# Optimization experiments

Measured on AMD Instinct MI355X. Metric: run time of the kernel, lower is better.

## Reference

```python
import jax, jax.numpy as jnp
import numpy as np

B, S, D_MODEL = 2, 1024, 3072
HEADS, HEAD_DIM = 24, 128
EPS = 1e-6


def _rms_norm(x, w):
    # RMSNorm over last dim (head_dim), elementwise affine
    var = jnp.mean(jnp.square(x), axis=-1, keepdims=True)
    return x * jax.lax.rsqrt(var + EPS) * w


def _apply_rotary(x, freqs_cis):
    # x: [B, S, H, D]; freqs_cis: [S, 1, rot_dim] broadcasting over B via leading dims
    rot_dim = freqs_cis.shape[-1]
    xr, x_pass = x[..., :rot_dim], x[..., rot_dim:]
    cos_ = jnp.cos(freqs_cis).astype(x.dtype)
    sin_ = jnp.sin(freqs_cis).astype(x.dtype)
    x1, x2 = jnp.split(xr, 2, axis=-1)
    x_rot = jnp.concatenate((-x2, x1), axis=-1)
    return jnp.concatenate((xr * cos_ + x_rot * sin_, x_pass), axis=-1)


def setup_inputs() -> dict:
    key = jax.random.key(0)
    ks = jax.random.split(key, 8)
    inner = HEADS * HEAD_DIM
    scale = 1.0 / np.sqrt(D_MODEL)
    return {
        "hidden_states": jax.random.normal(ks[0], (B, S, D_MODEL), dtype=jnp.float32),
        "image_rotary_emb": jax.random.uniform(ks[1], (S, 1, HEAD_DIM), dtype=jnp.float32) * 6.283,
        "Wq": jax.random.normal(ks[2], (inner, D_MODEL), dtype=jnp.float32) * scale,
        "Wk": jax.random.normal(ks[3], (inner, D_MODEL), dtype=jnp.float32) * scale,
        "Wv": jax.random.normal(ks[4], (inner, D_MODEL), dtype=jnp.float32) * scale,
        "Wo": jax.random.normal(ks[5], (D_MODEL, inner), dtype=jnp.float32) * scale,
        "norm_q_w": jnp.ones((HEAD_DIM,), dtype=jnp.float32),
        "norm_k_w": jnp.ones((HEAD_DIM,), dtype=jnp.float32),
    }


def reference(hidden_states, image_rotary_emb, Wq, Wk, Wv, Wo, norm_q_w, norm_k_w):
    # QKV projections: [B,S,Dm] @ [Dm,inner] -> [B,S,H,Dh]
    q = jnp.einsum("bsd,ed->bse", hidden_states, Wq).reshape(B, S, HEADS, HEAD_DIM)
    k = jnp.einsum("bsd,ed->bse", hidden_states, Wk).reshape(B, S, HEADS, HEAD_DIM)
    v = jnp.einsum("bsd,ed->bse", hidden_states, Wv).reshape(B, S, HEADS, HEAD_DIM)
    # per-head RMSNorm on q/k
    q = _rms_norm(q, norm_q_w)
    k = _rms_norm(k, norm_k_w)
    # RoPE (Megatron rotate_half, full head dim rotated)
    q = _apply_rotary(q, image_rotary_emb)
    k = _apply_rotary(k, image_rotary_emb)
    # SDPA (non-causal, no mask): [B,H,S,S]
    scale = 1.0 / np.sqrt(HEAD_DIM)
    scores = jnp.einsum("bqhd,bkhd->bhqk", q, k) * scale
    attn = jax.nn.softmax(scores, axis=-1)
    out = jnp.einsum("bhqk,bkhd->bqhd", attn, v).reshape(B, S, HEADS * HEAD_DIM)
    return jnp.einsum("bse,de->bsd", out, Wo)
```

## Files before the change

### kernel.cpp

```cpp
#include <hip/hip_runtime.h>
#include <hip/hip_bf16.h>
#include <math.h>

#define B_   2
#define S_   1024
#define DM_  3072
#define H_   24
#define HD_  128
#define BH_  (B_*H_)
#define KDIM 3072
#define QSCALE 0.08838834764831845f

typedef __attribute__((ext_vector_type(8))) short short8;
typedef __attribute__((ext_vector_type(4))) float f32x4;

__device__ __forceinline__ unsigned short f2bf(float f) {
    union { float f; unsigned u; } v; v.f = f;
    unsigned r = v.u + 0x7fffu + ((v.u >> 16) & 1u);
    return (unsigned short)(r >> 16);
}

#define GLD_LDS16(gptr, ldsptr)                                                            \
    __builtin_amdgcn_global_load_lds(                                                      \
        (const __attribute__((address_space(1))) unsigned int*)(gptr),                     \
        (__attribute__((address_space(3))) unsigned int*)(ldsptr), 16, 0, 0)

#define SEG0 1572864
#define SEGW 2359296
#define SB1  (SEG0 + SEGW)
#define SB2  (SB1 + SEGW)
#define SB3  (SB2 + SEGW)
#define SB4  (SB3 + SEGW)
#define SB5  (SB4 + 32768)
#define CVT_BLOCKS 43136

__global__ __launch_bounds__(256) void cvt_all(const float* __restrict__ hs,
                                               const float* __restrict__ Wq,
                                               const float* __restrict__ Wk,
                                               const float* __restrict__ Wv,
                                               const float* __restrict__ Wo,
                                               const float* __restrict__ freqs,
                                               unsigned short* __restrict__ Xb,
                                               unsigned short* __restrict__ Wqkvb,
                                               unsigned short* __restrict__ Wob,
                                               float2* __restrict__ tab) {
    int i = blockIdx.x * 256 + threadIdx.x;
    const float* src;
    unsigned short* dst;
    int j;
    if (i < SEG0)      { src = hs; dst = Xb;              j = i; }
    else if (i < SB1)  { src = Wq; dst = Wqkvb;           j = i - SEG0; }
    else if (i < SB2)  { src = Wk; dst = Wqkvb + 9437184; j = i - SB1; }
    else if (i < SB3)  { src = Wv; dst = Wqkvb + 18874368; j = i - SB2; }
    else if (i < SB4)  { src = Wo; dst = Wob;             j = i - SB3; }
    else {
        j = i - SB4;
        float4 f = ((const float4*)freqs)[j];
        float4 lo = make_float4(cosf(f.x), sinf(f.x), cosf(f.y), sinf(f.y));
        float4 hi = make_float4(cosf(f.z), sinf(f.z), cosf(f.w), sinf(f.w));
        ((float4*)tab)[2 * j]     = lo;
        ((float4*)tab)[2 * j + 1] = hi;
        return;
    }
    float4 v = ((const float4*)src)[j];
    ushort4 o;
    o.x = f2bf(v.x); o.y = f2bf(v.y); o.z = f2bf(v.z); o.w = f2bf(v.w);
    ((ushort4*)dst)[j] = o;
}

template <int FUSED>
__global__ __launch_bounds__(256) void gemm_fused(const unsigned short* __restrict__ A,
                                                  const unsigned short* __restrict__ Bm,
                                                  float* __restrict__ C, int Ndim,
                                                  const float2* __restrict__ rtab,
                                                  const float* __restrict__ nqw,
                                                  const float* __restrict__ nkw,
                                                  unsigned short* __restrict__ Qb,
                                                  unsigned short* __restrict__ Kb,
                                                  unsigned short* __restrict__ Vtb) {
    __shared__ __align__(16) unsigned short As[128 * 64];
    __shared__ __align__(16) unsigned short Bs[128 * 64];
    __shared__ float pse[4][64];
    const int t = threadIdx.x;
    const int bx = blockIdx.x;
    const int m0 = blockIdx.y * 128, n0 = bx * 128;
    const int w = t >> 6, lane = t & 63, quad = lane >> 4, ln = lane & 15;
    const int wm = (w >> 1) * 64;
    const int p = w & 1;
    const int dj0 = p ? 32 : 0;
    const int rl = lane >> 3;
    const int gc = (lane & 7) ^ rl;
    const int cs = ln & 7;
    const int woff = (w == 1) ? 32 : (w == 2) ? -32 : 0;

    f32x4 acc[4][4];
#pragma unroll
    for (int i = 0; i < 4; ++i)
#pragma unroll
        for (int j = 0; j < 4; ++j) acc[i][j] = (f32x4){0.f, 0.f, 0.f, 0.f};

    const unsigned short* ga = &A[(long long)(m0 + w * 32 + rl) * KDIM + gc * 8];
    const unsigned short* gb = &Bm[(long long)(n0 + w * 32 + woff + rl) * KDIM + gc * 8];

    for (int kt = 0; kt < KDIM / 64; ++kt) {
#pragma unroll
        for (int c = 0; c < 4; ++c) {
            const int r0 = w * 32 + c * 8;
            GLD_LDS16(ga + (long long)(c * 8) * KDIM, &As[r0 * 64]);
            GLD_LDS16(gb + (long long)(c * 8) * KDIM, &Bs[r0 * 64]);
        }
        ga += 64; gb += 64;
        __syncthreads();
#pragma unroll
        for (int ks = 0; ks < 2; ++ks) {
            short8 a[4], b[4];
#pragma unroll
            for (int i = 0; i < 4; ++i) {
                int row = wm + i * 16 + ln;
                a[i] = *(const short8*)&As[row * 64 + (((ks * 4 + quad) ^ cs) << 3)];
            }
#pragma unroll
            for (int j = 0; j < 4; ++j) {
                int row = p * 64 + j * 16 + ln;
                b[j] = *(const short8*)&Bs[row * 64 + (((ks * 4 + quad) ^ cs) << 3)];
            }
#pragma unroll
            for (int i = 0; i < 4; ++i)
#pragma unroll
                for (int j = 0; j < 4; ++j)
                    acc[i][j] = __builtin_amdgcn_mfma_f32_16x16x32_bf16(a[i], b[j], acc[i][j], 0, 0, 0);
        }
        __syncthreads();
    }

    if (!FUSED) {
#pragma unroll
        for (int i = 0; i < 4; ++i)
#pragma unroll
            for (int reg = 0; reg < 4; ++reg) {
                int row = m0 + wm + i * 16 + quad * 4 + reg;
                float* crow = C + (long long)row * Ndim + n0 + ln;
                crow[dj0]      = acc[i][0][reg];
                crow[dj0 + 16] = acc[i][1][reg];
                crow[dj0 + 64] = acc[i][2][reg];
                crow[dj0 + 80] = acc[i][3][reg];
            }
        return;
    }
    const int region = bx / 24;
    const int h = bx % 24;
    if (region < 2) {
#pragma unroll
        for (int i = 0; i < 4; ++i)
#pragma unroll
            for (int reg = 0; reg < 4; ++reg) {
                float s = 0.f;
#pragma unroll
                for (int j = 0; j < 4; ++j) { float v = acc[i][j][reg]; s += v * v; }
#pragma unroll
                for (int off = 8; off; off >>= 1) s += __shfl_xor(s, off, 16);
                if (ln == 0) pse[w][i * 16 + quad * 4 + reg] = s;
            }
        __syncthreads();
        const float* nw = region ? nkw : nqw;
        unsigned short* outp = region ? Kb : Qb;
        const float scl = region ? 1.f : QSCALE;
        const float nw0  = nw[dj0 + ln],      nw1  = nw[dj0 + 16 + ln];
        const float nw64 = nw[dj0 + 64 + ln], nw80 = nw[dj0 + 80 + ln];
#pragma unroll
        for (int i = 0; i < 4; ++i)
#pragma unroll
            for (int reg = 0; reg < 4; ++reg) {
                const int idx = i * 16 + quad * 4 + reg;
                const float tot = pse[w][idx] + pse[w ^ 1][idx];
                const float rr = rsqrtf(tot * (1.f / 128.f) + 1e-6f);
                const int row = m0 + wm + idx;
                const int b = row >> 10, s = row & 1023;
                const long long ob = ((long long)(b * H_ + h) * S_ + s) * HD_;
                {
                    const int d1 = dj0 + ln;
                    float y1 = acc[i][0][reg] * rr * nw0;
                    float y2 = acc[i][2][reg] * rr * nw64;
                    float2 c1 = rtab[s * HD_ + d1], c2 = rtab[s * HD_ + d1 + 64];
                    outp[ob + d1]      = f2bf((y1 * c1.x - y2 * c1.y) * scl);
                    outp[ob + d1 + 64] = f2bf((y2 * c2.x + y1 * c2.y) * scl);
                }
                {
                    const int d1 = dj0 + 16 + ln;
                    float y1 = acc[i][1][reg] * rr * nw1;
                    float y2 = acc[i][3][reg] * rr * nw80;
                    float2 c1 = rtab[s * HD_ + d1], c2 = rtab[s * HD_ + d1 + 64];
                    outp[ob + d1]      = f2bf((y1 * c1.x - y2 * c1.y) * scl);
                    outp[ob + d1 + 64] = f2bf((y2 * c2.x + y1 * c2.y) * scl);
                }
            }
    } else {
#pragma unroll
        for (int i = 0; i < 4; ++i)
#pragma unroll
            for (int reg = 0; reg < 4; ++reg) {
                const int row = m0 + wm + i * 16 + quad * 4 + reg;
                const int b = row >> 10, s = row & 1023;
                const long long vb = (long long)(b * H_ + h) * HD_;
#pragma unroll
                for (int j = 0; j < 4; ++j) {
                    const int d = dj0 + (j & 1) * 16 + (j >> 1) * 64 + ln;
                    Vtb[(vb + d) * S_ + s] = f2bf(acc[i][j][reg]);
                }
            }
    }
}

__global__ __launch_bounds__(256) void attn(const unsigned short* __restrict__ Qb,
                                            const unsigned short* __restrict__ Kb,
                                            const unsigned short* __restrict__ Vtb,
                                            unsigned short* __restrict__ Ob) {
    __shared__ __align__(16) unsigned short Ks[64 * 128];
    __shared__ __align__(16) unsigned short Vts[128 * 64];
    __shared__ __align__(16) unsigned short Ps[4][16][72];
    const int bh = blockIdx.x, qt = blockIdx.y;
    const int t = threadIdx.x, w = t >> 6, lane = t & 63, quad = lane >> 4, ln = lane & 15;
    const int b = bh / H_, h = bh - b * H_;

    short8 qfrag[4];
    const long long qbase = ((long long)bh * S_ + qt * 64 + w * 16 + ln) * HD_;
#pragma unroll
    for (int ks = 0; ks < 4; ++ks)
        qfrag[ks] = *(const short8*)&Qb[qbase + ks * 32 + quad * 8];

    f32x4 o[8];
#pragma unroll
    for (int n = 0; n < 8; ++n) o[n] = (f32x4){0.f, 0.f, 0.f, 0.f};
    float l_run[4] = {0.f, 0.f, 0.f, 0.f};

    const int krow_l = lane >> 4, ksl = lane & 15;
    const int vrow_l = lane >> 3, vsl = lane & 7;

    for (int kt = 0; kt < S_ / 64; ++kt) {
        __syncthreads();
#pragma unroll
        for (int c = 0; c < 4; ++c) {
            {
                const int r = c * 16 + w * 4 + krow_l;
                const int gcn = ksl ^ (r & 15);
                GLD_LDS16(&Kb[((long long)bh * S_ + kt * 64 + r) * HD_ + gcn * 8],
                          &Ks[(c * 16 + w * 4) * 128]);
            }
            {
                const int r = c * 32 + w * 8 + vrow_l;
                const int gcn = vsl ^ (r & 7);
                GLD_LDS16(&Vtb[((long long)bh * HD_ + r) * S_ + kt * 64 + gcn * 8],
                          &Vts[(c * 32 + w * 8) * 64]);
            }
        }
        __syncthreads();
        f32x4 sj[4];
#pragma unroll
        for (int j = 0; j < 4; ++j) {
            f32x4 sa = (f32x4){0.f, 0.f, 0.f, 0.f};
#pragma unroll
            for (int ks = 0; ks < 4; ++ks) {
                const int row = j * 16 + ln;
                const int slot = (ks * 4 + quad) ^ (row & 15);
                short8 bb = *(const short8*)&Ks[row * 128 + slot * 8];
                sa = __builtin_amdgcn_mfma_f32_16x16x32_bf16(qfrag[ks], bb, sa, 0, 0, 0);
            }
            sj[j] = sa;
        }
#pragma unroll
        for (int r = 0; r < 4; ++r) {
            float sum = 0.f;
#pragma unroll
            for (int j = 0; j < 4; ++j) {
                float p = __expf(sj[j][r]);
                sj[j][r] = p;
                sum += p;
            }
#pragma unroll
            for (int off = 8; off; off >>= 1) sum += __shfl_xor(sum, off, 16);
            l_run[r] += sum;
        }
#pragma unroll
        for (int j = 0; j < 4; ++j)
#pragma unroll
            for (int r = 0; r < 4; ++r)
                Ps[w][quad * 4 + r][j * 16 + ln] = f2bf(sj[j][r]);
        __asm__ volatile("s_waitcnt lgkmcnt(0)" ::: "memory");
#pragma unroll
        for (int ks = 0; ks < 2; ++ks) {
            short8 pf = *(const short8*)&Ps[w][ln][ks * 32 + quad * 8];
#pragma unroll
            for (int n = 0; n < 8; ++n) {
                const int row = n * 16 + ln;
                const int slot = (ks * 4 + quad) ^ (row & 7);
                short8 vf = *(const short8*)&Vts[row * 64 + slot * 8];
                o[n] = __builtin_amdgcn_mfma_f32_16x16x32_bf16(pf, vf, o[n], 0, 0, 0);
            }
        }
    }
    float inv[4];
#pragma unroll
    for (int r = 0; r < 4; ++r) inv[r] = 1.f / l_run[r];
    const int row_s = qt * 64 + w * 16 + quad * 4;
#pragma unroll
    for (int n = 0; n < 8; ++n)
#pragma unroll
        for (int r = 0; r < 4; ++r) {
            long long off = ((long long)b * S_ + row_s + r) * DM_ + h * HD_ + n * 16 + ln;
            Ob[off] = f2bf(o[n][r] * inv[r]);
        }
}

extern "C" void kernel_launch(void* const* d_in, const int* in_sizes, int n_in,
                              void* d_out, int out_size, void* d_ws, size_t ws_size,
                              hipStream_t stream) {
    const float* hs    = (const float*)d_in[0];
    const float* freqs = (const float*)d_in[1];
    const float* Wq    = (const float*)d_in[2];
    const float* Wk    = (const float*)d_in[3];
    const float* Wv    = (const float*)d_in[4];
    const float* Wo    = (const float*)d_in[5];
    const float* nqw   = (const float*)d_in[6];
    const float* nkw   = (const float*)d_in[7];
    float* out = (float*)d_out;

    char* ws = (char*)d_ws;
    unsigned short* Xb    = (unsigned short*)(ws);
    unsigned short* Wqkvb = (unsigned short*)(ws + 12582912LL);
    unsigned short* Wob   = (unsigned short*)(ws + 69206016LL);
    unsigned short* Qb    = (unsigned short*)(ws + 88080384LL);
    unsigned short* Kb    = (unsigned short*)(ws + 100663296LL);
    unsigned short* Vtb   = (unsigned short*)(ws + 113246208LL);
    unsigned short* Ob    = (unsigned short*)(ws + 125829120LL);
    float2*         rtab  = (float2*)        (ws + 138412032LL);

    cvt_all<<<CVT_BLOCKS, 256, 0, stream>>>(hs, Wq, Wk, Wv, Wo, freqs,
                                            Xb, Wqkvb, Wob, rtab);
    gemm_fused<1><<<dim3(72, 16), 256, 0, stream>>>(Xb, Wqkvb, nullptr, 0,
                                                    rtab, nqw, nkw, Qb, Kb, Vtb);
    attn<<<dim3(BH_, S_ / 64), 256, 0, stream>>>(Qb, Kb, Vtb, Ob);
    gemm_fused<0><<<dim3(24, 16), 256, 0, stream>>>(Ob, Wob, out, DM_,
                                                    nullptr, nullptr, nullptr,
                                                    nullptr, nullptr, nullptr);
}
```

Before: 459.5 us.

## Double-buffer attention K/V tiles and stage GEMM epilogue stores through LDS

The attention kernel now double-buffers its K and V^T shared-memory tiles. It issues the async global-to-LDS loads for the next key tile before computing on the current one, and raises wave priority around the MFMA sections. The QKV GEMM epilogue writes normalized and rotated Q/K, and transposed V, into a swizzled LDS tile that reuses the GEMM's staging memory. It then emits coalesced 16-byte global stores instead of scattered 2-byte stores, the V^T layout being the worst case. The cost is doubled attention LDS footprint, which may lower occupancy, and an extra barrier. In the V path the reuse of shared memory has no barrier before the writes, so it depends on all warps having finished reading the GEMM tiles.

After: 466.3 us. About the same (+1.5%).

```diff
diff --git a/kernel.cpp b/kernel.cpp
--- a/kernel.cpp
+++ b/kernel.cpp
@@ -78,9 +78,10 @@
                                                   unsigned short* __restrict__ Qb,
                                                   unsigned short* __restrict__ Kb,
                                                   unsigned short* __restrict__ Vtb) {
-    __shared__ __align__(16) unsigned short As[128 * 64];
-    __shared__ __align__(16) unsigned short Bs[128 * 64];
+    __shared__ __align__(16) unsigned short smem[128 * 128];
     __shared__ float pse[4][64];
+    unsigned short* const As = smem;
+    unsigned short* const Bs = smem + 128 * 64;
     const int t = threadIdx.x;
     const int bx = blockIdx.x;
     const int m0 = blockIdx.y * 128, n0 = bx * 128;
@@ -149,6 +150,10 @@
     }
     const int region = bx / 24;
     const int h = bx % 24;
+    unsigned short* const Ct = smem;
+    const int bb  = m0 >> 10;
+    const int s0g = m0 & 1023;
+
     if (region < 2) {
 #pragma unroll
         for (int i = 0; i < 4; ++i)
@@ -174,40 +179,56 @@
                 const int idx = i * 16 + quad * 4 + reg;
                 const float tot = pse[w][idx] + pse[w ^ 1][idx];
                 const float rr = rsqrtf(tot * (1.f / 128.f) + 1e-6f);
-                const int row = m0 + wm + idx;
-                const int b = row >> 10, s = row & 1023;
-                const long long ob = ((long long)(b * H_ + h) * S_ + s) * HD_;
+                const int rloc = wm + idx;
+                const int s = s0g + rloc;
+                const int sw = (rloc & 15) << 3;
                 {
                     const int d1 = dj0 + ln;
                     float y1 = acc[i][0][reg] * rr * nw0;
                     float y2 = acc[i][2][reg] * rr * nw64;
                     float2 c1 = rtab[s * HD_ + d1], c2 = rtab[s * HD_ + d1 + 64];
-                    outp[ob + d1]      = f2bf((y1 * c1.x - y2 * c1.y) * scl);
-                    outp[ob + d1 + 64] = f2bf((y2 * c2.x + y1 * c2.y) * scl);
+                    Ct[rloc * 128 + (d1 ^ sw)]        = f2bf((y1 * c1.x - y2 * c1.y) * scl);
+                    Ct[rloc * 128 + ((d1 + 64) ^ sw)] = f2bf((y2 * c2.x + y1 * c2.y) * scl);
                 }
                 {
                     const int d1 = dj0 + 16 + ln;
                     float y1 = acc[i][1][reg] * rr * nw1;
                     float y2 = acc[i][3][reg] * rr * nw80;
                     float2 c1 = rtab[s * HD_ + d1], c2 = rtab[s * HD_ + d1 + 64];
-                    outp[ob + d1]      = f2bf((y1 * c1.x - y2 * c1.y) * scl);
-                    outp[ob + d1 + 64] = f2bf((y2 * c2.x + y1 * c2.y) * scl);
+                    Ct[rloc * 128 + (d1 ^ sw)]        = f2bf((y1 * c1.x - y2 * c1.y) * scl);
+                    Ct[rloc * 128 + ((d1 + 64) ^ sw)] = f2bf((y2 * c2.x + y1 * c2.y) * scl);
                 }
             }
+        __syncthreads();
+        const long long obase = (long long)(bb * H_ + h) * S_ + s0g;
+#pragma unroll
+        for (int ps = 0; ps < 8; ++ps) {
+            const int rloc = ps * 16 + (t >> 4);
+            const int ch   = (t & 15) ^ (t >> 4);
+            short8 vv = *(const short8*)&Ct[rloc * 128 + ch * 8];
+            *(short8*)&outp[(obase + rloc) * HD_ + (t & 15) * 8] = vv;
+        }
     } else {
 #pragma unroll
         for (int i = 0; i < 4; ++i)
 #pragma unroll
             for (int reg = 0; reg < 4; ++reg) {
-                const int row = m0 + wm + i * 16 + quad * 4 + reg;
-                const int b = row >> 10, s = row & 1023;
-                const long long vb = (long long)(b * H_ + h) * HD_;
+                const int sl = wm + i * 16 + quad * 4 + reg;
 #pragma unroll
                 for (int j = 0; j < 4; ++j) {
                     const int d = dj0 + (j & 1) * 16 + (j >> 1) * 64 + ln;
-                    Vtb[(vb + d) * S_ + s] = f2bf(acc[i][j][reg]);
+                    Ct[d * 128 + (sl ^ ((d & 15) << 3))] = f2bf(acc[i][j][reg]);
                 }
             }
+        __syncthreads();
+        const long long vb = (long long)(bb * H_ + h) * HD_;
+#pragma unroll
+        for (int ps = 0; ps < 8; ++ps) {
+            const int dr = ps * 16 + (t >> 4);
+            const int ch = (t & 15) ^ (t >> 4);
+            short8 vv = *(const short8*)&Ct[dr * 128 + ch * 8];
+            *(short8*)&Vtb[(vb + dr) * S_ + s0g + (t & 15) * 8] = vv;
+        }
     }
 }
 
@@ -215,8 +236,8 @@
                                             const unsigned short* __restrict__ Kb,
                                             const unsigned short* __restrict__ Vtb,
                                             unsigned short* __restrict__ Ob) {
-    __shared__ __align__(16) unsigned short Ks[64 * 128];
-    __shared__ __align__(16) unsigned short Vts[128 * 64];
+    __shared__ __align__(16) unsigned short Ks[2][64 * 128];
+    __shared__ __align__(16) unsigned short Vts[2][128 * 64];
     __shared__ __align__(16) unsigned short Ps[4][16][72];
     const int bh = blockIdx.x, qt = blockIdx.y;
     const int t = threadIdx.x, w = t >> 6, lane = t & 63, quad = lane >> 4, ln = lane & 15;
@@ -235,26 +256,29 @@
 
     const int krow_l = lane >> 4, ksl = lane & 15;
     const int vrow_l = lane >> 3, vsl = lane & 7;
+    const long long kbase = (long long)bh * S_ * HD_;
+    const long long vbase = (long long)bh * HD_ * S_;
+
+#define ATTN_STAGE(buf, ktile) do {                                                        \
+    _Pragma("unroll")                                                                      \
+    for (int c = 0; c < 4; ++c) {                                                          \
+        const int rk = c * 16 + w * 4 + krow_l;                                            \
+        GLD_LDS16(&Kb[kbase + ((long long)((ktile) * 64 + rk)) * HD_ + (ksl ^ (rk & 15)) * 8], \
+                  &Ks[buf][(c * 16 + w * 4) * 128]);                                       \
+        const int rv = c * 32 + w * 8 + vrow_l;                                            \
+        GLD_LDS16(&Vtb[vbase + (long long)rv * S_ + (ktile) * 64 + (vsl ^ (rv & 7)) * 8],  \
+                  &Vts[buf][(c * 32 + w * 8) * 64]);                                       \
+    } } while (0)
+
+    ATTN_STAGE(0, 0);
+    __syncthreads();
 
     for (int kt = 0; kt < S_ / 64; ++kt) {
-        __syncthreads();
-#pragma unroll
-        for (int c = 0; c < 4; ++c) {
-            {
-                const int r = c * 16 + w * 4 + krow_l;
-                const int gcn = ksl ^ (r & 15);
-                GLD_LDS16(&Kb[((long long)bh * S_ + kt * 64 + r) * HD_ + gcn * 8],
-                          &Ks[(c * 16 + w * 4) * 128]);
-            }
-            {
-                const int r = c * 32 + w * 8 + vrow_l;
-                const int gcn = vsl ^ (r & 7);
-                GLD_LDS16(&Vtb[((long long)bh * HD_ + r) * S_ + kt * 64 + gcn * 8],
-                          &Vts[(c * 32 + w * 8) * 64]);
-            }
-        }
-        __syncthreads();
+        const int cur = kt & 1;
+        if (kt + 1 < S_ / 64) ATTN_STAGE(cur ^ 1, kt + 1);
+
         f32x4 sj[4];
+        __builtin_amdgcn_s_setprio(1);
 #pragma unroll
         for (int j = 0; j < 4; ++j) {
             f32x4 sa = (f32x4){0.f, 0.f, 0.f, 0.f};
@@ -262,11 +286,12 @@
             for (int ks = 0; ks < 4; ++ks) {
                 const int row = j * 16 + ln;
                 const int slot = (ks * 4 + quad) ^ (row & 15);
-                short8 bb = *(const short8*)&Ks[row * 128 + slot * 8];
-                sa = __builtin_amdgcn_mfma_f32_16x16x32_bf16(qfrag[ks], bb, sa, 0, 0, 0);
+                short8 kb = *(const short8*)&Ks[cur][row * 128 + slot * 8];
+                sa = __builtin_amdgcn_mfma_f32_16x16x32_bf16(qfrag[ks], kb, sa, 0, 0, 0);
             }
             sj[j] = sa;
         }
+        __builtin_amdgcn_s_setprio(0);
 #pragma unroll
         for (int r = 0; r < 4; ++r) {
             float sum = 0.f;
@@ -286,6 +311,7 @@
             for (int r = 0; r < 4; ++r)
                 Ps[w][quad * 4 + r][j * 16 + ln] = f2bf(sj[j][r]);
         __asm__ volatile("s_waitcnt lgkmcnt(0)" ::: "memory");
+        __builtin_amdgcn_s_setprio(1);
 #pragma unroll
         for (int ks = 0; ks < 2; ++ks) {
             short8 pf = *(const short8*)&Ps[w][ln][ks * 32 + quad * 8];
@@ -293,11 +319,15 @@
             for (int n = 0; n < 8; ++n) {
                 const int row = n * 16 + ln;
                 const int slot = (ks * 4 + quad) ^ (row & 7);
-                short8 vf = *(const short8*)&Vts[row * 64 + slot * 8];
+                short8 vf = *(const short8*)&Vts[cur][row * 64 + slot * 8];
                 o[n] = __builtin_amdgcn_mfma_f32_16x16x32_bf16(pf, vf, o[n], 0, 0, 0);
             }
         }
-    }
+        __builtin_amdgcn_s_setprio(0);
+        __syncthreads();
+    }
+#undef ATTN_STAGE
+
     float inv[4];
 #pragma unroll
     for (int r = 0; r < 4; ++r) inv[r] = 1.f / l_run[r];
```

## Load attention K/V fragments directly from global memory, drop LDS staging

Applied to the files above, without the earlier changes.

The attention kernel no longer stages K and V^T tiles into shared memory with global_load_lds and block barriers. Each wave now reads its MFMA B-operand fragments straight from global memory, relying on L1/L2 to serve the reuse across the four waves. s_setprio hints are also added around the MFMA sections. This removes the two barriers per iteration and the LDS traffic, but every wave now issues redundant global loads and exposes their latency with no prefetching.

New measurement: 577.7 us. 25.7% more time.

```diff
diff --git a/kernel.cpp b/kernel.cpp
--- a/kernel.cpp
+++ b/kernel.cpp
@@ -215,8 +215,6 @@
                                             const unsigned short* __restrict__ Kb,
                                             const unsigned short* __restrict__ Vtb,
                                             unsigned short* __restrict__ Ob) {
-    __shared__ __align__(16) unsigned short Ks[64 * 128];
-    __shared__ __align__(16) unsigned short Vts[128 * 64];
     __shared__ __align__(16) unsigned short Ps[4][16][72];
     const int bh = blockIdx.x, qt = blockIdx.y;
     const int t = threadIdx.x, w = t >> 6, lane = t & 63, quad = lane >> 4, ln = lane & 15;
@@ -233,40 +231,26 @@
     for (int n = 0; n < 8; ++n) o[n] = (f32x4){0.f, 0.f, 0.f, 0.f};
     float l_run[4] = {0.f, 0.f, 0.f, 0.f};
 
-    const int krow_l = lane >> 4, ksl = lane & 15;
-    const int vrow_l = lane >> 3, vsl = lane & 7;
+    const unsigned short* kp = Kb + (long long)bh * S_ * HD_;
+    const unsigned short* vp = Vtb + (long long)bh * HD_ * S_;
 
     for (int kt = 0; kt < S_ / 64; ++kt) {
-        __syncthreads();
-#pragma unroll
-        for (int c = 0; c < 4; ++c) {
-            {
-                const int r = c * 16 + w * 4 + krow_l;
-                const int gcn = ksl ^ (r & 15);
-                GLD_LDS16(&Kb[((long long)bh * S_ + kt * 64 + r) * HD_ + gcn * 8],
-                          &Ks[(c * 16 + w * 4) * 128]);
-            }
-            {
-                const int r = c * 32 + w * 8 + vrow_l;
-                const int gcn = vsl ^ (r & 7);
-                GLD_LDS16(&Vtb[((long long)bh * HD_ + r) * S_ + kt * 64 + gcn * 8],
-                          &Vts[(c * 32 + w * 8) * 64]);
-            }
-        }
-        __syncthreads();
+        const unsigned short* ktp = kp + (long long)kt * 64 * HD_;
+        const unsigned short* vtp = vp + kt * 64;
+
         f32x4 sj[4];
+        __builtin_amdgcn_s_setprio(1);
 #pragma unroll
         for (int j = 0; j < 4; ++j) {
             f32x4 sa = (f32x4){0.f, 0.f, 0.f, 0.f};
 #pragma unroll
             for (int ks = 0; ks < 4; ++ks) {
-                const int row = j * 16 + ln;
-                const int slot = (ks * 4 + quad) ^ (row & 15);
-                short8 bb = *(const short8*)&Ks[row * 128 + slot * 8];
-                sa = __builtin_amdgcn_mfma_f32_16x16x32_bf16(qfrag[ks], bb, sa, 0, 0, 0);
+                short8 kb = *(const short8*)&ktp[(j * 16 + ln) * HD_ + ks * 32 + quad * 8];
+                sa = __builtin_amdgcn_mfma_f32_16x16x32_bf16(qfrag[ks], kb, sa, 0, 0, 0);
             }
             sj[j] = sa;
         }
+        __builtin_amdgcn_s_setprio(0);
 #pragma unroll
         for (int r = 0; r < 4; ++r) {
             float sum = 0.f;
@@ -286,18 +270,19 @@
             for (int r = 0; r < 4; ++r)
                 Ps[w][quad * 4 + r][j * 16 + ln] = f2bf(sj[j][r]);
         __asm__ volatile("s_waitcnt lgkmcnt(0)" ::: "memory");
+        __builtin_amdgcn_s_setprio(1);
 #pragma unroll
         for (int ks = 0; ks < 2; ++ks) {
             short8 pf = *(const short8*)&Ps[w][ln][ks * 32 + quad * 8];
 #pragma unroll
             for (int n = 0; n < 8; ++n) {
-                const int row = n * 16 + ln;
-                const int slot = (ks * 4 + quad) ^ (row & 7);
-                short8 vf = *(const short8*)&Vts[row * 64 + slot * 8];
+                short8 vf = *(const short8*)&vtp[(long long)(n * 16 + ln) * S_ + ks * 32 + quad * 8];
                 o[n] = __builtin_amdgcn_mfma_f32_16x16x32_bf16(pf, vf, o[n], 0, 0, 0);
             }
         }
-    }
+        __builtin_amdgcn_s_setprio(0);
+    }
+
     float inv[4];
 #pragma unroll
     for (int r = 0; r < 4; ++r) inv[r] = 1.f / l_run[r];
```
